# Kernel tuning notes

Measured on AMD Instinct MI355X. Metric: run time of the kernel, lower is better.

The kernel has to match this reference:

```python
import jax, jax.numpy as jnp
import numpy as np

B, S, E, H = 4, 2048, 1024, 16
D = E // H  # head_dim = 64

def setup_inputs() -> dict:
    key = jax.random.key(0)
    k1, k2, k3, k4, k5 = jax.random.split(key, 5)
    x = jax.random.normal(k1, (B, S, E), dtype=jnp.float32)
    # causal mask, broadcast over batch and heads; mask==0 -> -inf
    mask = jnp.tril(jnp.ones((S, S), dtype=jnp.int32))[None, None, :, :]
    Wqkv = jax.random.normal(k2, (E, 3 * E), dtype=jnp.float32) * (1.0 / np.sqrt(E))
    bqkv = jax.random.normal(k3, (3 * E,), dtype=jnp.float32) * 0.02
    Wo = jax.random.normal(k4, (E, E), dtype=jnp.float32) * (1.0 / np.sqrt(E))
    bo = jax.random.normal(k5, (E,), dtype=jnp.float32) * 0.02
    return {"x": x, "mask": mask, "Wqkv": Wqkv, "bqkv": bqkv, "Wo": Wo, "bo": bo}

def reference(x, mask, Wqkv, bqkv, Wo, bo):
    b, s, e = x.shape
    scale = 1.0 / np.sqrt(D)
    qkv = x @ Wqkv + bqkv                      # [b,s,3e]
    qkv = qkv.reshape(b, s, H, 3 * D).transpose(0, 2, 1, 3)  # [b,h,s,3d]
    q, k, v = jnp.split(qkv, 3, axis=-1)       # each [b,h,s,d]
    scores = jnp.einsum('bnqd,bnkd->bnqk', q, k) * scale
    scores = jnp.where(mask == 0, -jnp.inf, scores)
    probs = jax.nn.softmax(scores, axis=-1)
    attn = jnp.einsum('bnqk,bnkd->bnqd', probs, v)  # [b,h,s,d]
    # Faithful to source: reshape (b,h,s,d) -> (b,s,e) WITHOUT transposing back
    attn = attn.reshape(b, s, e)
    return attn @ Wo + bo
```

## Files before the change

kernel.cpp:

```cpp
#include <hip/hip_runtime.h>

typedef __attribute__((ext_vector_type(8))) short bf16x8;
typedef __attribute__((ext_vector_type(4))) float f32x4;
typedef __attribute__((ext_vector_type(2))) unsigned int u32x2;
typedef __attribute__((ext_vector_type(4))) unsigned int u32x4;

#define MFMA16(a, b, c) __builtin_amdgcn_mfma_f32_16x16x32_bf16((a), (b), (c), 0, 0, 0)

#define S_LEN 2048
#define NHEAD 16
#define DHEAD 64
#define BH    64
#define MROWS 8192

__device__ __forceinline__ unsigned short f2bf(float f) {
  unsigned int u = __builtin_bit_cast(unsigned int, f);
  u += 0x7FFFu + ((u >> 16) & 1u);
  return (unsigned short)(u >> 16);
}

__device__ __forceinline__ void gl_lds16(const void* g, void* l) {
  __builtin_amdgcn_global_load_lds(
      (const __attribute__((address_space(1))) void*)g,
      (__attribute__((address_space(3))) void*)l, 16, 0, 0);
}

__device__ __forceinline__ unsigned int pkbf(float lo, float hi) {
  unsigned int ulo = __builtin_bit_cast(unsigned int, lo) + 0x8000u;
  unsigned int uhi = __builtin_bit_cast(unsigned int, hi) + 0x8000u;
  return __builtin_amdgcn_perm(uhi, ulo, 0x07060302u);
}

__global__ __launch_bounds__(256) void cast_bf16(const float* __restrict__ src,
                                                 unsigned short* __restrict__ dst, int n) {
  int i = (blockIdx.x * 256 + threadIdx.x) * 4;
  if (i + 3 < n) {
    f32x4 v = *(const f32x4*)(src + i);
    unsigned long long pk =
        (unsigned long long)f2bf(v[0]) |
        ((unsigned long long)f2bf(v[1]) << 16) |
        ((unsigned long long)f2bf(v[2]) << 32) |
        ((unsigned long long)f2bf(v[3]) << 48);
    *(unsigned long long*)(dst + i) = pk;
  }
}

__global__ __launch_bounds__(256) void transpose_cast(const float* __restrict__ src,
                                                      unsigned short* __restrict__ dst,
                                                      int R, int C) {
  __shared__ float tile[32][33];
  int c0 = blockIdx.x * 32, r0 = blockIdx.y * 32;
  int tx = threadIdx.x, ty = threadIdx.y;
  for (int i = 0; i < 32; i += 8)
    tile[ty + i][tx] = src[(size_t)(r0 + ty + i) * C + c0 + tx];
  __syncthreads();
  for (int i = 0; i < 32; i += 8)
    dst[(size_t)(c0 + ty + i) * R + r0 + tx] = f2bf(tile[tx][ty + i]);
}

__global__ __launch_bounds__(256) void transpose_cast_qkv(const float* __restrict__ src,
                                                          unsigned short* __restrict__ dst) {
  __shared__ float tile[32][33];
  int c0 = blockIdx.x * 32, r0 = blockIdx.y * 32;
  int tx = threadIdx.x, ty = threadIdx.y;
  for (int i = 0; i < 32; i += 8)
    tile[ty + i][tx] = src[(size_t)(r0 + ty + i) * 3072 + c0 + tx];
  __syncthreads();
  for (int i = 0; i < 32; i += 8) {
    int oc = c0 + ty + i;
    int h = oc / 192, rr = oc % 192;
    int nc = ((rr >> 6) << 10) + (h << 6) + (rr & 63);
    dst[(size_t)nc * 1024 + r0 + tx] = f2bf(tile[tx][ty + i]);
  }
}

#define GEMM_CORE(A_, Bt_)                                                              \
  __shared__ unsigned short As[128 * 32];                                               \
  __shared__ unsigned short Bs[128 * 32];                                               \
  const int tid = threadIdx.x;                                                          \
  const int w = tid >> 6, lane = tid & 63, l15 = lane & 15, quad = lane >> 4;           \
  const int wm = w >> 1, wn = w & 1;                                                    \
  const int col0 = blockIdx.x * 128, row0 = blockIdx.y * 128;                           \
  f32x4 acc[4][4] = {};                                                                 \
  for (int kt = 0; kt < 32; ++kt) {                                                     \
    const int k0 = kt * 32;                                                             \
    for (int p = 0; p < 2; ++p) {                                                       \
      int c = p * 256 + tid;                                                            \
      int m = c >> 2, k8 = (c & 3) * 8;                                                 \
      void* ldsA = (char*)As + (size_t)(p * 256 + (tid & 192)) * 16;                    \
      void* ldsB = (char*)Bs + (size_t)(p * 256 + (tid & 192)) * 16;                    \
      gl_lds16(A_ + (size_t)(row0 + m) * 1024 + k0 + k8, ldsA);                         \
      gl_lds16(Bt_ + (size_t)(col0 + m) * 1024 + k0 + k8, ldsB);                        \
    }                                                                                   \
    __syncthreads();                                                                    \
    bf16x8 af[4], bfr[4];                                                               \
    for (int i = 0; i < 4; ++i)                                                         \
      af[i] = *(const bf16x8*)&As[(wm * 64 + i * 16 + l15) * 32 + quad * 8];            \
    for (int j = 0; j < 4; ++j)                                                         \
      bfr[j] = *(const bf16x8*)&Bs[(wn * 64 + j * 16 + l15) * 32 + quad * 8];           \
    for (int i = 0; i < 4; ++i)                                                         \
      for (int j = 0; j < 4; ++j)                                                       \
        acc[i][j] = MFMA16(af[i], bfr[j], acc[i][j]);                                   \
    __syncthreads();                                                                    \
  }

__global__ __launch_bounds__(256) void gemm_qkv(const unsigned short* __restrict__ A,
                                                const unsigned short* __restrict__ Bt,
                                                const float* __restrict__ bias,
                                                unsigned short* __restrict__ Qb,
                                                unsigned short* __restrict__ Kb,
                                                unsigned short* __restrict__ Vtb) {
  __shared__ float Es[32][132];
  GEMM_CORE(A, Bt)
  const int bx = col0 >> 7;
  float bv[4];
  #pragma unroll
  for (int j = 0; j < 4; ++j) {
    int nc = col0 + wn * 64 + j * 16 + l15;
    int oc = ((nc >> 6) & 15) * 192 + (nc >> 10) * 64 + (nc & 63);
    bv[j] = bias[oc];
  }
  const float sc = (bx < 8) ? 0.18033688011112042f : 1.0f;
  const int b = row0 >> 11;
  for (int i = 0; i < 4; ++i) {
    __syncthreads();
    #pragma unroll
    for (int j = 0; j < 4; ++j)
      #pragma unroll
      for (int r = 0; r < 4; ++r)
        Es[wm * 16 + quad * 4 + r][wn * 64 + j * 16 + l15] = (acc[i][j][r] + bv[j]) * sc;
    __syncthreads();
    if (bx < 16) {
      int lr = tid >> 3, ch = tid & 7;
      int grow = row0 + (lr >> 4) * 64 + i * 16 + (lr & 15);
      int s = grow & 2047;
      int nc0 = col0 + ch * 16;
      int h = (nc0 >> 6) & 15, d0 = nc0 & 63;
      const float* ep = &Es[lr][ch * 16];
      f32x4 v0 = *(const f32x4*)ep, v1 = *(const f32x4*)(ep + 4);
      f32x4 v2 = *(const f32x4*)(ep + 8), v3 = *(const f32x4*)(ep + 12);
      u32x4 pk0 = {pkbf(v0[0], v0[1]), pkbf(v0[2], v0[3]), pkbf(v1[0], v1[1]), pkbf(v1[2], v1[3])};
      u32x4 pk1 = {pkbf(v2[0], v2[1]), pkbf(v2[2], v2[3]), pkbf(v3[0], v3[1]), pkbf(v3[2], v3[3])};
      unsigned short* dst = (bx < 8 ? Qb : Kb) + ((size_t)(b * 16 + h) * 2048 + s) * 64 + d0;
      *(u32x4*)dst = pk0;
      *(u32x4*)(dst + 8) = pk1;
    } else {
      int grp = tid >> 7, c = tid & 127;
      int s0 = (row0 & 2047) + grp * 64 + i * 16;
      int nc = col0 + c;
      int h = (nc >> 6) & 15, d = nc & 63;
      float e[16];
      #pragma unroll
      for (int k = 0; k < 16; ++k) e[k] = Es[grp * 16 + k][c];
      u32x4 pk0 = {pkbf(e[0], e[1]), pkbf(e[2], e[3]), pkbf(e[4], e[5]), pkbf(e[6], e[7])};
      u32x4 pk1 = {pkbf(e[8], e[9]), pkbf(e[10], e[11]), pkbf(e[12], e[13]), pkbf(e[14], e[15])};
      unsigned short* dst = Vtb + ((size_t)(b * 16 + h) * 64 + d) * 2048 + s0;
      *(u32x4*)dst = pk0;
      *(u32x4*)(dst + 8) = pk1;
    }
  }
}

__global__ __launch_bounds__(256) void gemm_out(const unsigned short* __restrict__ A,
                                                const unsigned short* __restrict__ Bt,
                                                const float* __restrict__ bias,
                                                float* __restrict__ out) {
  GEMM_CORE(A, Bt)
  for (int i = 0; i < 4; ++i) {
    int grow = row0 + wm * 64 + i * 16 + quad * 4;
    for (int j = 0; j < 4; ++j) {
      int gcol = col0 + wn * 64 + j * 16 + l15;
      float bvv = bias[gcol];
      for (int r = 0; r < 4; ++r)
        out[(size_t)(grow + r) * 1024 + gcol] = acc[i][j][r] + bvv;
    }
  }
}

__global__ __launch_bounds__(256) void attn_kernel(const unsigned short* __restrict__ Qb,
                                                   const unsigned short* __restrict__ Kb,
                                                   const unsigned short* __restrict__ Vtb,
                                                   unsigned short* __restrict__ attnout) {
  __shared__ unsigned short K0[64 * 32], K1[64 * 32];
  __shared__ unsigned short V0[64 * 32], V1[64 * 32];
  __shared__ unsigned short P0[4][2][512], P1[4][2][512];

  const int tid = threadIdx.x;
  const int w = tid >> 6, lane = tid & 63, l15 = lane & 15, quad = lane >> 4;
  const int qt = 15 - (blockIdx.x >> 6);
  const int bh = blockIdx.x & 63;
  const int q0w = qt * 128 + w * 32;

  const unsigned short* Qg = Qb + (size_t)bh * S_LEN * DHEAD;
  const unsigned short* Kg = Kb + (size_t)bh * S_LEN * DHEAD;
  const unsigned short* Vg = Vtb + (size_t)bh * DHEAD * S_LEN;

  bf16x8 qf[2][2];
  #pragma unroll
  for (int sub = 0; sub < 2; ++sub) {
    const unsigned short* p = Qg + (size_t)(q0w + sub * 16 + l15) * DHEAD + quad * 8;
    qf[sub][0] = *(const bf16x8*)p;
    qf[sub][1] = *(const bf16x8*)(p + 32);
  }

  const int srow = tid >> 2, sc8 = (tid & 3) * 8;
  const unsigned short* kgb = Kg + srow * 64 + sc8;
  const unsigned short* vgb = Vg + (size_t)srow * S_LEN + sc8;
  const int wKo = srow * 32 + sc8;

  const int psw = (l15 & 3) ^ ((l15 >> 2) & 3);
  const int pw0 = l15 * 32 + (((quad >> 1) ^ psw) << 3) + ((quad & 1) << 2);
  const int pw1 = l15 * 32 + (((2 + (quad >> 1)) ^ psw) << 3) + ((quad & 1) << 2);
  const int pro = l15 * 32 + ((quad ^ psw) << 3);
  const int kvo = l15 * 32 + quad * 8;

  f32x4 oacc[2][4] = {};
  f32x4 lsum[2] = {};
  const bf16x8 ones = {0x3F80, 0x3F80, 0x3F80, 0x3F80, 0x3F80, 0x3F80, 0x3F80, 0x3F80};

  const int ktfull = 2 * qt;
  const int nkt = ktfull + 2;

  bf16x8 kr0 = *(const bf16x8*)kgb, kr1 = *(const bf16x8*)(kgb + 32);
  bf16x8 vr0 = *(const bf16x8*)vgb, vr1 = *(const bf16x8*)(vgb + 32);

  for (int kt = 0; kt < nkt; ++kt) {
    *(bf16x8*)&K0[wKo] = kr0;  *(bf16x8*)&K1[wKo] = kr1;
    *(bf16x8*)&V0[wKo] = vr0;  *(bf16x8*)&V1[wKo] = vr1;
    __syncthreads();
    if (kt + 1 < nkt) {
      const unsigned short* kp = kgb + (kt + 1) * 4096;
      const unsigned short* vp = vgb + (kt + 1) * 64;
      kr0 = *(const bf16x8*)kp;  kr1 = *(const bf16x8*)(kp + 32);
      vr0 = *(const bf16x8*)vp;  vr1 = *(const bf16x8*)(vp + 32);
    }

    const bool pB = (kt == ktfull + 1);
    const bool act = !pB || (w >= 2);
    unsigned short* pda0 = P0[w][0];  unsigned short* pdb0 = P1[w][0];
    unsigned short* pda1 = P0[w][1];  unsigned short* pdb1 = P1[w][1];

    if (kt < ktfull) {
      f32x4 st[2][4];
      #pragma unroll
      for (int jk = 0; jk < 4; ++jk) {
        bf16x8 kf0 = *(const bf16x8*)&K0[jk * 512 + kvo];
        bf16x8 kf1 = *(const bf16x8*)&K1[jk * 512 + kvo];
        f32x4 z0 = {}, z1 = {};
        z0 = MFMA16(kf0, qf[0][0], z0);  z0 = MFMA16(kf1, qf[0][1], z0);
        z1 = MFMA16(kf0, qf[1][0], z1);  z1 = MFMA16(kf1, qf[1][1], z1);
        st[0][jk] = z0;  st[1][jk] = z1;
      }
      #pragma unroll
      for (int sub = 0; sub < 2; ++sub) {
        unsigned short* pda = sub ? pda1 : pda0;
        unsigned short* pdb = sub ? pdb1 : pdb0;
        #pragma unroll
        for (int jk = 0; jk < 4; ++jk) {
          float e0 = __builtin_amdgcn_exp2f(st[sub][jk][0]);
          float e1 = __builtin_amdgcn_exp2f(st[sub][jk][1]);
          float e2 = __builtin_amdgcn_exp2f(st[sub][jk][2]);
          float e3 = __builtin_amdgcn_exp2f(st[sub][jk][3]);
          u32x2 pk2 = {pkbf(e0, e1), pkbf(e2, e3)};
          *(u32x2*)&((jk < 2) ? pda : pdb)[(jk & 1) ? pw1 : pw0] = pk2;
        }
      }
    } else if (act) {
      const int jmax = pB ? (2 * w - 3) : (2 * w + 1);
      f32x4 st[2][4];
      #pragma unroll
      for (int jk = 0; jk < 4; ++jk) {
        if (jk <= jmax) {
          bf16x8 kf0 = *(const bf16x8*)&K0[jk * 512 + kvo];
          bf16x8 kf1 = *(const bf16x8*)&K1[jk * 512 + kvo];
          f32x4 z0 = {}, z1 = {};
          z0 = MFMA16(kf0, qf[0][0], z0);  z0 = MFMA16(kf1, qf[0][1], z0);
          z1 = MFMA16(kf0, qf[1][0], z1);  z1 = MFMA16(kf1, qf[1][1], z1);
          st[0][jk] = z0;  st[1][jk] = z1;
        }
      }
      #pragma unroll
      for (int sub = 0; sub < 2; ++sub) {
        const int jklim = jmax - 1 + sub;
        unsigned short* pda = sub ? pda1 : pda0;
        unsigned short* pdb = sub ? pdb1 : pdb0;
        #pragma unroll
        for (int jk = 0; jk < 4; ++jk) {
          unsigned int* dst = (unsigned int*)&((jk < 2) ? pda : pdb)[(jk & 1) ? pw1 : pw0];
          if (jk > jklim) {
            *(u32x2*)dst = (u32x2){0u, 0u};
          } else {
            f32x4 z = st[sub][jk];
            if (jk == jklim) {
              #pragma unroll
              for (int r = 0; r < 4; ++r)
                if (quad * 4 + r > l15) z[r] = -3e38f;
            }
            float e0 = __builtin_amdgcn_exp2f(z[0]);
            float e1 = __builtin_amdgcn_exp2f(z[1]);
            float e2 = __builtin_amdgcn_exp2f(z[2]);
            float e3 = __builtin_amdgcn_exp2f(z[3]);
            *(u32x2*)dst = (u32x2){pkbf(e0, e1), pkbf(e2, e3)};
          }
        }
      }
    }

    if (act) {
      bf16x8 pf[2][2];
      pf[0][0] = *(const bf16x8*)&pda0[pro];  pf[0][1] = *(const bf16x8*)&pdb0[pro];
      pf[1][0] = *(const bf16x8*)&pda1[pro];  pf[1][1] = *(const bf16x8*)&pdb1[pro];
      lsum[0] = MFMA16(pf[0][0], ones, lsum[0]);
      lsum[0] = MFMA16(pf[0][1], ones, lsum[0]);
      lsum[1] = MFMA16(pf[1][0], ones, lsum[1]);
      lsum[1] = MFMA16(pf[1][1], ones, lsum[1]);
      #pragma unroll
      for (int dt = 0; dt < 4; ++dt) {
        bf16x8 vb0 = *(const bf16x8*)&V0[dt * 512 + kvo];
        bf16x8 vb1 = *(const bf16x8*)&V1[dt * 512 + kvo];
        oacc[0][dt] = MFMA16(pf[0][0], vb0, oacc[0][dt]);
        oacc[0][dt] = MFMA16(pf[0][1], vb1, oacc[0][dt]);
        oacc[1][dt] = MFMA16(pf[1][0], vb0, oacc[1][dt]);
        oacc[1][dt] = MFMA16(pf[1][1], vb1, oacc[1][dt]);
      }
    }
    __syncthreads();
  }

  #pragma unroll
  for (int sub = 0; sub < 2; ++sub) {
    #pragma unroll
    for (int r = 0; r < 4; ++r) {
      float inv = __builtin_amdgcn_rcpf(lsum[sub][r]);
      int row = q0w + sub * 16 + quad * 4 + r;
      unsigned short* dst = attnout + ((size_t)bh * S_LEN + row) * DHEAD;
      #pragma unroll
      for (int dt = 0; dt < 4; ++dt)
        dst[dt * 16 + l15] = f2bf(oacc[sub][dt][r] * inv);
    }
  }
}

extern "C" void kernel_launch(void* const* d_in, const int* in_sizes, int n_in,
                              void* d_out, int out_size, void* d_ws, size_t ws_size,
                              hipStream_t stream) {
  const float* x    = (const float*)d_in[0];
  const float* Wqkv = (const float*)d_in[2];
  const float* bqkv = (const float*)d_in[3];
  const float* Wo   = (const float*)d_in[4];
  const float* bo   = (const float*)d_in[5];
  float* out = (float*)d_out;

  char* ws = (char*)d_ws;
  unsigned short* Xbf   = (unsigned short*)(ws);
  unsigned short* WqkvT = (unsigned short*)(ws + 16777216);
  unsigned short* WoT   = (unsigned short*)(ws + 23068672);
  unsigned short* Qb    = (unsigned short*)(ws + 25165824);
  unsigned short* Kb    = (unsigned short*)(ws + 41943040);
  unsigned short* Vtb   = (unsigned short*)(ws + 58720256);
  unsigned short* Attn  = (unsigned short*)(ws + 75497472);

  cast_bf16<<<8192, 256, 0, stream>>>(x, Xbf, MROWS * 1024);
  transpose_cast_qkv<<<dim3(96, 32), dim3(32, 8), 0, stream>>>(Wqkv, WqkvT);
  transpose_cast<<<dim3(32, 32), dim3(32, 8), 0, stream>>>(Wo, WoT, 1024, 1024);
  gemm_qkv<<<dim3(24, 64), 256, 0, stream>>>(Xbf, WqkvT, bqkv, Qb, Kb, Vtb);
  attn_kernel<<<1024, 256, 0, stream>>>(Qb, Kb, Vtb, Attn);
  gemm_out<<<dim3(8, 64), 256, 0, stream>>>(Attn, WoT, bo, out);
}
```

Before: 280.6 us.

## Double attention query tile per block, sum softmax denominators in registers, per-wave epilogue

The attention kernel now handles 256 query rows per block (64 per wave) instead of 128, so each K/V tile staged in LDS is reused by twice as many queries and the grid halves to 512 blocks. Query tiles are interleaved to balance causal work. The softmax denominator is now accumulated in registers from the exp values and reduced with shuffles, replacing the extra MFMAs against a ones vector. The QKV GEMM epilogue stages through a per-wave LDS scratch region, which removes block-wide barriers. The changes cost more registers, fewer blocks for load balance, and wave idling on the diagonal tiles.

```diff
diff --git a/kernel.cpp b/kernel.cpp
--- a/kernel.cpp
+++ b/kernel.cpp
@@ -110,7 +110,7 @@
                                                 unsigned short* __restrict__ Qb,
                                                 unsigned short* __restrict__ Kb,
                                                 unsigned short* __restrict__ Vtb) {
-  __shared__ float Es[32][132];
+  __shared__ float Es[4][16][66];
   GEMM_CORE(A, Bt)
   const int bx = col0 >> 7;
   float bv[4];
@@ -122,39 +122,44 @@
   }
   const float sc = (bx < 8) ? 0.18033688011112042f : 1.0f;
   const int b = row0 >> 11;
-  for (int i = 0; i < 4; ++i) {
-    __syncthreads();
-    #pragma unroll
-    for (int j = 0; j < 4; ++j)
-      #pragma unroll
-      for (int r = 0; r < 4; ++r)
-        Es[wm * 16 + quad * 4 + r][wn * 64 + j * 16 + l15] = (acc[i][j][r] + bv[j]) * sc;
-    __syncthreads();
-    if (bx < 16) {
-      int lr = tid >> 3, ch = tid & 7;
-      int grow = row0 + (lr >> 4) * 64 + i * 16 + (lr & 15);
-      int s = grow & 2047;
-      int nc0 = col0 + ch * 16;
-      int h = (nc0 >> 6) & 15, d0 = nc0 & 63;
-      const float* ep = &Es[lr][ch * 16];
-      f32x4 v0 = *(const f32x4*)ep, v1 = *(const f32x4*)(ep + 4);
-      f32x4 v2 = *(const f32x4*)(ep + 8), v3 = *(const f32x4*)(ep + 12);
-      u32x4 pk0 = {pkbf(v0[0], v0[1]), pkbf(v0[2], v0[3]), pkbf(v1[0], v1[1]), pkbf(v1[2], v1[3])};
-      u32x4 pk1 = {pkbf(v2[0], v2[1]), pkbf(v2[2], v2[3]), pkbf(v3[0], v3[1]), pkbf(v3[2], v3[3])};
-      unsigned short* dst = (bx < 8 ? Qb : Kb) + ((size_t)(b * 16 + h) * 2048 + s) * 64 + d0;
+  const int srow0 = (row0 & 2047) + wm * 64;
+  const int h = ((col0 + wn * 64) >> 6) & 15;
+  float (*Ew)[66] = Es[w];
+
+  if (bx < 16) {
+    const int lr = lane >> 2, ch2 = lane & 3, d0 = ch2 * 16;
+    unsigned short* base = (bx < 8 ? Qb : Kb) + ((size_t)(b * 16 + h) * 2048) * 64;
+    for (int i = 0; i < 4; ++i) {
+      #pragma unroll
+      for (int j = 0; j < 4; ++j)
+        #pragma unroll
+        for (int r = 0; r < 4; ++r)
+          Ew[quad * 4 + r][j * 16 + l15] = (acc[i][j][r] + bv[j]) * sc;
+      float v[16];
+      #pragma unroll
+      for (int c = 0; c < 4; ++c)
+        *(f32x4*)&v[4 * c] = *(const f32x4*)&Ew[lr][d0 + 4 * c];
+      u32x4 pk0 = {pkbf(v[0], v[1]), pkbf(v[2], v[3]), pkbf(v[4], v[5]), pkbf(v[6], v[7])};
+      u32x4 pk1 = {pkbf(v[8], v[9]), pkbf(v[10], v[11]), pkbf(v[12], v[13]), pkbf(v[14], v[15])};
+      unsigned short* dst = base + (size_t)(srow0 + i * 16 + lr) * 64 + d0;
       *(u32x4*)dst = pk0;
       *(u32x4*)(dst + 8) = pk1;
-    } else {
-      int grp = tid >> 7, c = tid & 127;
-      int s0 = (row0 & 2047) + grp * 64 + i * 16;
-      int nc = col0 + c;
-      int h = (nc >> 6) & 15, d = nc & 63;
+    }
+  } else {
+    const int d = lane;
+    unsigned short* base = Vtb + ((size_t)(b * 16 + h) * 64 + d) * 2048;
+    for (int i = 0; i < 4; ++i) {
+      #pragma unroll
+      for (int j = 0; j < 4; ++j)
+        #pragma unroll
+        for (int r = 0; r < 4; ++r)
+          Ew[quad * 4 + r][j * 16 + l15] = acc[i][j][r] + bv[j];
       float e[16];
       #pragma unroll
-      for (int k = 0; k < 16; ++k) e[k] = Es[grp * 16 + k][c];
+      for (int k = 0; k < 16; ++k) e[k] = Ew[k][d];
       u32x4 pk0 = {pkbf(e[0], e[1]), pkbf(e[2], e[3]), pkbf(e[4], e[5]), pkbf(e[6], e[7])};
       u32x4 pk1 = {pkbf(e[8], e[9]), pkbf(e[10], e[11]), pkbf(e[12], e[13]), pkbf(e[14], e[15])};
-      unsigned short* dst = Vtb + ((size_t)(b * 16 + h) * 64 + d) * 2048 + s0;
+      unsigned short* dst = base + srow0 + i * 16;
       *(u32x4*)dst = pk0;
       *(u32x4*)(dst + 8) = pk1;
     }
@@ -183,21 +188,24 @@
                                                    unsigned short* __restrict__ attnout) {
   __shared__ unsigned short K0[64 * 32], K1[64 * 32];
   __shared__ unsigned short V0[64 * 32], V1[64 * 32];
-  __shared__ unsigned short P0[4][2][512], P1[4][2][512];
+  __shared__ unsigned short P0[4][4][512], P1[4][4][512];
+  __shared__ float Lbc[4][64];
 
   const int tid = threadIdx.x;
   const int w = tid >> 6, lane = tid & 63, l15 = lane & 15, quad = lane >> 4;
-  const int qt = 15 - (blockIdx.x >> 6);
+  const int i2 = blockIdx.x >> 6;
+  const int jj = ((i2 & 1) << 1) | ((i2 >> 1) & 1);
+  const int qt = (i2 & 4) ? jj : 7 - jj;
   const int bh = blockIdx.x & 63;
-  const int q0w = qt * 128 + w * 32;
+  const int q0w = qt * 256 + w * 64;
 
   const unsigned short* Qg = Qb + (size_t)bh * S_LEN * DHEAD;
   const unsigned short* Kg = Kb + (size_t)bh * S_LEN * DHEAD;
   const unsigned short* Vg = Vtb + (size_t)bh * DHEAD * S_LEN;
 
-  bf16x8 qf[2][2];
+  bf16x8 qf[4][2];
   #pragma unroll
-  for (int sub = 0; sub < 2; ++sub) {
+  for (int sub = 0; sub < 4; ++sub) {
     const unsigned short* p = Qg + (size_t)(q0w + sub * 16 + l15) * DHEAD + quad * 8;
     qf[sub][0] = *(const bf16x8*)p;
     qf[sub][1] = *(const bf16x8*)(p + 32);
@@ -210,16 +218,15 @@
 
   const int psw = (l15 & 3) ^ ((l15 >> 2) & 3);
   const int pw0 = l15 * 32 + (((quad >> 1) ^ psw) << 3) + ((quad & 1) << 2);
-  const int pw1 = l15 * 32 + (((2 + (quad >> 1)) ^ psw) << 3) + ((quad & 1) << 2);
+  const int pw1 = l15 * 32 + ((((quad >> 1) + 2) ^ psw) << 3) + ((quad & 1) << 2);
   const int pro = l15 * 32 + ((quad ^ psw) << 3);
   const int kvo = l15 * 32 + quad * 8;
 
-  f32x4 oacc[2][4] = {};
-  f32x4 lsum[2] = {};
-  const bf16x8 ones = {0x3F80, 0x3F80, 0x3F80, 0x3F80, 0x3F80, 0x3F80, 0x3F80, 0x3F80};
-
-  const int ktfull = 2 * qt;
-  const int nkt = ktfull + 2;
+  f32x4 oacc[4][4] = {};
+  float lacc[4] = {0.f, 0.f, 0.f, 0.f};
+
+  const int ktdiag = 4 * qt;
+  const int nkt = ktdiag + 4;
 
   bf16x8 kr0 = *(const bf16x8*)kgb, kr1 = *(const bf16x8*)(kgb + 32);
   bf16x8 vr0 = *(const bf16x8*)vgb, vr1 = *(const bf16x8*)(vgb + 32);
@@ -235,63 +242,44 @@
       vr0 = *(const bf16x8*)vp;  vr1 = *(const bf16x8*)(vp + 32);
     }
 
-    const bool pB = (kt == ktfull + 1);
-    const bool act = !pB || (w >= 2);
-    unsigned short* pda0 = P0[w][0];  unsigned short* pdb0 = P1[w][0];
-    unsigned short* pda1 = P0[w][1];  unsigned short* pdb1 = P1[w][1];
-
-    if (kt < ktfull) {
-      f32x4 st[2][4];
-      #pragma unroll
-      for (int jk = 0; jk < 4; ++jk) {
-        bf16x8 kf0 = *(const bf16x8*)&K0[jk * 512 + kvo];
-        bf16x8 kf1 = *(const bf16x8*)&K1[jk * 512 + kvo];
-        f32x4 z0 = {}, z1 = {};
-        z0 = MFMA16(kf0, qf[0][0], z0);  z0 = MFMA16(kf1, qf[0][1], z0);
-        z1 = MFMA16(kf0, qf[1][0], z1);  z1 = MFMA16(kf1, qf[1][1], z1);
-        st[0][jk] = z0;  st[1][jk] = z1;
-      }
-      #pragma unroll
-      for (int sub = 0; sub < 2; ++sub) {
-        unsigned short* pda = sub ? pda1 : pda0;
-        unsigned short* pdb = sub ? pdb1 : pdb0;
+    const int t = kt - ktdiag;
+    const bool act = (t < 0) || (w >= t);
+
+    if (act) {
+      if (t < 0) {
         #pragma unroll
         for (int jk = 0; jk < 4; ++jk) {
-          float e0 = __builtin_amdgcn_exp2f(st[sub][jk][0]);
-          float e1 = __builtin_amdgcn_exp2f(st[sub][jk][1]);
-          float e2 = __builtin_amdgcn_exp2f(st[sub][jk][2]);
-          float e3 = __builtin_amdgcn_exp2f(st[sub][jk][3]);
-          u32x2 pk2 = {pkbf(e0, e1), pkbf(e2, e3)};
-          *(u32x2*)&((jk < 2) ? pda : pdb)[(jk & 1) ? pw1 : pw0] = pk2;
-        }
-      }
-    } else if (act) {
-      const int jmax = pB ? (2 * w - 3) : (2 * w + 1);
-      f32x4 st[2][4];
-      #pragma unroll
-      for (int jk = 0; jk < 4; ++jk) {
-        if (jk <= jmax) {
           bf16x8 kf0 = *(const bf16x8*)&K0[jk * 512 + kvo];
           bf16x8 kf1 = *(const bf16x8*)&K1[jk * 512 + kvo];
-          f32x4 z0 = {}, z1 = {};
-          z0 = MFMA16(kf0, qf[0][0], z0);  z0 = MFMA16(kf1, qf[0][1], z0);
-          z1 = MFMA16(kf0, qf[1][0], z1);  z1 = MFMA16(kf1, qf[1][1], z1);
-          st[0][jk] = z0;  st[1][jk] = z1;
+          #pragma unroll
+          for (int sub = 0; sub < 4; ++sub) {
+            f32x4 z = {};
+            z = MFMA16(kf0, qf[sub][0], z);
+            z = MFMA16(kf1, qf[sub][1], z);
+            float e0 = __builtin_amdgcn_exp2f(z[0]);
+            float e1 = __builtin_amdgcn_exp2f(z[1]);
+            float e2 = __builtin_amdgcn_exp2f(z[2]);
+            float e3 = __builtin_amdgcn_exp2f(z[3]);
+            lacc[sub] += (e0 + e1) + (e2 + e3);
+            unsigned short* pd = (jk < 2) ? P0[w][sub] : P1[w][sub];
+            *(u32x2*)&pd[(jk & 1) ? pw1 : pw0] = (u32x2){pkbf(e0, e1), pkbf(e2, e3)};
+          }
         }
-      }
-      #pragma unroll
-      for (int sub = 0; sub < 2; ++sub) {
-        const int jklim = jmax - 1 + sub;
-        unsigned short* pda = sub ? pda1 : pda0;
-        unsigned short* pdb = sub ? pdb1 : pdb0;
+      } else {
+        const bool dg = (t == w);
         #pragma unroll
         for (int jk = 0; jk < 4; ++jk) {
-          unsigned int* dst = (unsigned int*)&((jk < 2) ? pda : pdb)[(jk & 1) ? pw1 : pw0];
-          if (jk > jklim) {
-            *(u32x2*)dst = (u32x2){0u, 0u};
-          } else {
-            f32x4 z = st[sub][jk];
-            if (jk == jklim) {
+          bf16x8 kf0 = *(const bf16x8*)&K0[jk * 512 + kvo];
+          bf16x8 kf1 = *(const bf16x8*)&K1[jk * 512 + kvo];
+          #pragma unroll
+          for (int sub = 0; sub < 4; ++sub) {
+            unsigned short* pd = (jk < 2) ? P0[w][sub] : P1[w][sub];
+            unsigned int* dst = (unsigned int*)&pd[(jk & 1) ? pw1 : pw0];
+            if (dg && jk > sub) { *(u32x2*)dst = (u32x2){0u, 0u}; continue; }
+            f32x4 z = {};
+            z = MFMA16(kf0, qf[sub][0], z);
+            z = MFMA16(kf1, qf[sub][1], z);
+            if (dg && jk == sub) {
               #pragma unroll
               for (int r = 0; r < 4; ++r)
                 if (quad * 4 + r > l15) z[r] = -3e38f;
@@ -300,43 +288,50 @@
             float e1 = __builtin_amdgcn_exp2f(z[1]);
             float e2 = __builtin_amdgcn_exp2f(z[2]);
             float e3 = __builtin_amdgcn_exp2f(z[3]);
+            lacc[sub] += (e0 + e1) + (e2 + e3);
             *(u32x2*)dst = (u32x2){pkbf(e0, e1), pkbf(e2, e3)};
           }
         }
       }
-    }
-
-    if (act) {
-      bf16x8 pf[2][2];
-      pf[0][0] = *(const bf16x8*)&pda0[pro];  pf[0][1] = *(const bf16x8*)&pdb0[pro];
-      pf[1][0] = *(const bf16x8*)&pda1[pro];  pf[1][1] = *(const bf16x8*)&pdb1[pro];
-      lsum[0] = MFMA16(pf[0][0], ones, lsum[0]);
-      lsum[0] = MFMA16(pf[0][1], ones, lsum[0]);
-      lsum[1] = MFMA16(pf[1][0], ones, lsum[1]);
-      lsum[1] = MFMA16(pf[1][1], ones, lsum[1]);
+
+      bf16x8 pf[4][2];
+      #pragma unroll
+      for (int sub = 0; sub < 4; ++sub) {
+        pf[sub][0] = *(const bf16x8*)&P0[w][sub][pro];
+        pf[sub][1] = *(const bf16x8*)&P1[w][sub][pro];
+      }
       #pragma unroll
       for (int dt = 0; dt < 4; ++dt) {
         bf16x8 vb0 = *(const bf16x8*)&V0[dt * 512 + kvo];
         bf16x8 vb1 = *(const bf16x8*)&V1[dt * 512 + kvo];
-        oacc[0][dt] = MFMA16(pf[0][0], vb0, oacc[0][dt]);
-        oacc[0][dt] = MFMA16(pf[0][1], vb1, oacc[0][dt]);
-        oacc[1][dt] = MFMA16(pf[1][0], vb0, oacc[1][dt]);
-        oacc[1][dt] = MFMA16(pf[1][1], vb1, oacc[1][dt]);
+        #pragma unroll
+        for (int sub = 0; sub < 4; ++sub) {
+          oacc[sub][dt] = MFMA16(pf[sub][0], vb0, oacc[sub][dt]);
+          oacc[sub][dt] = MFMA16(pf[sub][1], vb1, oacc[sub][dt]);
+        }
       }
     }
     __syncthreads();
   }
 
   #pragma unroll
-  for (int sub = 0; sub < 2; ++sub) {
+  for (int sub = 0; sub < 4; ++sub) {
+    float l = lacc[sub];
+    l += __shfl_xor(l, 16);
+    l += __shfl_xor(l, 32);
+    if (quad == 0) Lbc[w][sub * 16 + l15] = l;
+  }
+  #pragma unroll
+  for (int sub = 0; sub < 4; ++sub) {
+    f32x4 l4 = *(const f32x4*)&Lbc[w][sub * 16 + quad * 4];
+    int qbase = q0w + sub * 16 + quad * 4;
+    unsigned short* dst = attnout + ((size_t)bh * S_LEN + qbase) * DHEAD;
     #pragma unroll
     for (int r = 0; r < 4; ++r) {
-      float inv = __builtin_amdgcn_rcpf(lsum[sub][r]);
-      int row = q0w + sub * 16 + quad * 4 + r;
-      unsigned short* dst = attnout + ((size_t)bh * S_LEN + row) * DHEAD;
+      float inv = __builtin_amdgcn_rcpf(l4[r]);
       #pragma unroll
       for (int dt = 0; dt < 4; ++dt)
-        dst[dt * 16 + l15] = f2bf(oacc[sub][dt][r] * inv);
+        dst[(size_t)r * DHEAD + dt * 16 + l15] = f2bf(oacc[sub][dt][r] * inv);
     }
   }
 }
@@ -364,6 +359,6 @@
   transpose_cast_qkv<<<dim3(96, 32), dim3(32, 8), 0, stream>>>(Wqkv, WqkvT);
   transpose_cast<<<dim3(32, 32), dim3(32, 8), 0, stream>>>(Wo, WoT, 1024, 1024);
   gemm_qkv<<<dim3(24, 64), 256, 0, stream>>>(Xbf, WqkvT, bqkv, Qb, Kb, Vtb);
-  attn_kernel<<<1024, 256, 0, stream>>>(Qb, Kb, Vtb, Attn);
+  attn_kernel<<<512, 256, 0, stream>>>(Qb, Kb, Vtb, Attn);
   gemm_out<<<dim3(8, 64), 256, 0, stream>>>(Attn, WoT, bo, out);
 }
```

Result: faster. 267.0 us (-4.8%).
